# Kernel optimization log

Hardware: AMD Instinct MI355X
Metric: run time of the kernel (lower is better)

Reference implementation:

```python
import jax, jax.numpy as jnp
import numpy as np

B, S, H, R = 32, 512, 1024, 64


def _bernoulli(key, shape, p=0.05):
    return (jax.random.uniform(key, shape) < p).astype(jnp.float32)


def setup_inputs() -> dict:
    key = jax.random.key(0)
    ks = jax.random.split(key, 16)
    context = jax.random.normal(ks[0], (B, S, H), dtype=jnp.float32)
    masks = jnp.ones((B, S), dtype=jnp.float32)
    all_subject_heads = _bernoulli(ks[1], (B, S))
    all_subject_tails = _bernoulli(ks[2], (B, S))
    # one-hot subject head/tail positions (tail >= head)
    h_pos = jax.random.randint(ks[3], (B,), 0, S // 2)
    t_pos = h_pos + jax.random.randint(ks[4], (B,), 0, 8)
    subject_head = jax.nn.one_hot(h_pos, S, dtype=jnp.float32)
    subject_tail = jax.nn.one_hot(t_pos, S, dtype=jnp.float32)
    object_heads = _bernoulli(ks[5], (B, S, R))
    object_tails = _bernoulli(ks[6], (B, S, R))
    # learned parameters (PyTorch Linear: y = x @ W.T + b; store as [in, out])
    sc = 1.0 / np.sqrt(H)
    Ws_h = jax.random.uniform(ks[7], (H, 1), minval=-sc, maxval=sc)
    bs_h = jnp.zeros((1,), dtype=jnp.float32)
    Ws_t = jax.random.uniform(ks[8], (H, 1), minval=-sc, maxval=sc)
    bs_t = jnp.zeros((1,), dtype=jnp.float32)
    Wo_h = jax.random.uniform(ks[9], (H, R), minval=-sc, maxval=sc)
    bo_h = jnp.zeros((R,), dtype=jnp.float32)
    Wo_t = jax.random.uniform(ks[10], (H, R), minval=-sc, maxval=sc)
    bo_t = jnp.zeros((R,), dtype=jnp.float32)
    return dict(context=context, masks=masks,
                all_subject_heads=all_subject_heads, all_subject_tails=all_subject_tails,
                subject_head=subject_head, subject_tail=subject_tail,
                object_heads=object_heads, object_tails=object_tails,
                Ws_h=Ws_h, bs_h=bs_h, Ws_t=Ws_t, bs_t=bs_t,
                Wo_h=Wo_h, bo_h=bo_h, Wo_t=Wo_t, bo_t=bo_t)


def _bce_with_logits(logits, targets):
    # numerically stable, matches F.binary_cross_entropy_with_logits(reduction='none')
    return jnp.maximum(logits, 0.0) - logits * targets + jnp.log1p(jnp.exp(-jnp.abs(logits)))


def _masked_loss(gold, pred, mask):
    loss = _bce_with_logits(pred, gold)
    if loss.ndim != mask.ndim:
        mask = mask[..., None]
    return jnp.sum(loss * mask) / jnp.sum(mask)


def reference(context, masks, all_subject_heads, all_subject_tails,
              subject_head, subject_tail, object_heads, object_tails,
              Ws_h, bs_h, Ws_t, bs_t, Wo_h, bo_h, Wo_t, bo_t):
    # subject logits: [B,S]
    pred_subject_heads = (context @ Ws_h + bs_h)[..., 0]
    pred_subject_tails = (context @ Ws_t + bs_t)[..., 0]
    # subject pooling: one-hot [B,S] x context [B,S,H] -> [B,H]
    sub_h = jnp.einsum('bs,bsh->bh', subject_head, context)
    sub_t = jnp.einsum('bs,bsh->bh', subject_tail, context)
    subject = (sub_h + sub_t) * 0.5
    context_subject = context + subject[:, None, :]  # [B,S,H]
    pred_object_heads = context_subject @ Wo_h + bo_h  # [B,S,R]
    pred_object_tails = context_subject @ Wo_t + bo_t  # [B,S,R]
    loss = (_masked_loss(all_subject_heads, pred_subject_heads, masks)
            + _masked_loss(all_subject_tails, pred_subject_tails, masks)
            + _masked_loss(object_heads, pred_object_heads, masks)
            + _masked_loss(object_tails, pred_object_tails, masks))
    return loss
```

## Files before the change

### kernel.cpp

```cpp
#include <hip/hip_runtime.h>
#include <hip/hip_bf16.h>


#define B_  32
#define S_  512
#define H_  1024
#define R_  64
#define M_  (B_ * S_)
#define NPAD 160
#define NVALID 130
#define BK 64
#define BKP 72
#define MT 32

typedef __attribute__((ext_vector_type(4))) float  floatx4;
typedef __attribute__((ext_vector_type(8))) short  short8;
typedef __attribute__((ext_vector_type(4))) unsigned short u16x4;
typedef __attribute__((ext_vector_type(8))) unsigned short u16x8;

__device__ __forceinline__ unsigned short f2bf(float f) {
    unsigned int u = __float_as_uint(f);
    u = (u + 0x7FFFu + ((u >> 16) & 1u)) >> 16;
    return (unsigned short)u;
}
__device__ __forceinline__ float bf2f(unsigned short h) {
    return __uint_as_float(((unsigned int)h) << 16);
}

__global__ void prep_weights(const float* __restrict__ Wo_h,
                             const float* __restrict__ Wo_t,
                             const float* __restrict__ Ws_h,
                             const float* __restrict__ Ws_t,
                             unsigned short* __restrict__ WtG) {
    int n = blockIdx.x;
    int tid = threadIdx.x;
    for (int k = tid; k < H_; k += 256) {
        float v;
        if (n < 64)        v = Wo_h[k * R_ + n];
        else if (n < 128)  v = Wo_t[k * R_ + (n - 64)];
        else if (n == 128) v = Ws_h[k];
        else if (n == 129) v = Ws_t[k];
        else               v = 0.0f;
        WtG[n * H_ + k] = f2bf(v);
    }
}

__global__ __launch_bounds__(256) void subj_kernel(
        const float* __restrict__ ctx, const float* __restrict__ head,
        const float* __restrict__ tail, const float* __restrict__ masks,
        const float* __restrict__ Wo_h, const float* __restrict__ Wo_t,
        const float* __restrict__ bo_h, const float* __restrict__ bo_t,
        const float* __restrict__ bs_h, const float* __restrict__ bs_t,
        float* __restrict__ rowBias, float* __restrict__ accum) {
    int b = blockIdx.x, tid = threadIdx.x;
    __shared__ float subj[H_];
    __shared__ int cnt;
    __shared__ int   sidx[8];
    __shared__ float sw[8];
    if (tid == 0) cnt = 0;
    __syncthreads();
    float msk = 0.0f;
    for (int s = tid; s < S_; s += 256) {
        float w = 0.5f * (head[b * S_ + s] + tail[b * S_ + s]);
        if (w != 0.0f) {
            int i = atomicAdd(&cnt, 1);
            if (i < 8) { sidx[i] = s; sw[i] = w; }
        }
        msk += masks[b * S_ + s];
    }
    for (int o = 32; o > 0; o >>= 1) msk += __shfl_down(msk, o, 64);
    if ((tid & 63) == 0) atomicAdd(&accum[1], msk);
    __syncthreads();
    int nnz = cnt < 8 ? cnt : 8;
    for (int h = tid; h < H_; h += 256) {
        float a = 0.0f;
        for (int i = 0; i < nnz; i++)
            a += sw[i] * ctx[((size_t)b * S_ + sidx[i]) * H_ + h];
        subj[h] = a;
    }
    __syncthreads();
    if (tid < NPAD) {
        float bias = tid < 64  ? bo_h[tid]
                   : tid < 128 ? bo_t[tid - 64]
                   : tid == 128 ? bs_h[0]
                   : tid == 129 ? bs_t[0] : 0.0f;
        float acc2 = 0.0f;
        if (tid < 128) {
            const float* W = (tid < 64) ? Wo_h : Wo_t;
            int c = tid & 63;
            for (int k = 0; k < H_; k++) acc2 += subj[k] * W[k * R_ + c];
        }
        rowBias[b * NPAD + tid] = bias + acc2;
    }
}

__global__ __launch_bounds__(256, 2) void main_kernel(
        const float* __restrict__ ctx, const unsigned short* __restrict__ WtG,
        const float* __restrict__ rowBias, const float* __restrict__ masks,
        const float* __restrict__ ash, const float* __restrict__ ast,
        const float* __restrict__ oh, const float* __restrict__ ot,
        float* __restrict__ accum) {
    __shared__ __align__(16) unsigned short Asm[MT * BKP];
    __shared__ __align__(16) unsigned short Bsm[NPAD * BKP];
    __shared__ float rbuf[4];

    const int tid = threadIdx.x;
    const int bm = blockIdx.x;
    const int gm0 = bm * MT;
    const int b = gm0 >> 9;
    const int wave = tid >> 6, lane = tid & 63;
    const int wm = wave & 1;
    const int wn = wave >> 1;
    const int lr = lane & 15, q = lane >> 4;

    const int ar = tid >> 4, af = tid & 15;
    const int bn = tid >> 3, bf = tid & 7;
    const float* aSrc0 = ctx + (size_t)(gm0 + ar) * H_ + af * 4;
    const unsigned short* bSrc0 = WtG + bn * H_ + bf * 8;
    unsigned short* aDst0 = &Asm[ar * BKP + af * 4];
    unsigned short* bDst0 = &Bsm[bn * BKP + bf * 8];

    const int aOff = (wm * 16 + lr) * BKP + q * 8;
    const int bOffBase = (wn * 80 + lr) * BKP + q * 8;

    floatx4 acc[5];
#pragma unroll
    for (int t = 0; t < 5; t++) acc[t] = (floatx4){0.f, 0.f, 0.f, 0.f};

    for (int k0 = 0; k0 < H_; k0 += BK) {
        __syncthreads();
#pragma unroll
        for (int ii = 0; ii < 2; ii++) {
            const float4 v = *(const float4*)(aSrc0 + ii * 16 * H_ + k0);
            u16x4 u = { f2bf(v.x), f2bf(v.y), f2bf(v.z), f2bf(v.w) };
            *(u16x4*)(aDst0 + ii * 16 * BKP) = u;
        }
#pragma unroll
        for (int ii = 0; ii < 5; ii++) {
            u16x8 w = *(const u16x8*)(bSrc0 + ii * 32 * H_ + k0);
            *(u16x8*)(bDst0 + ii * 32 * BKP) = w;
        }
        __syncthreads();
#pragma unroll
        for (int kk = 0; kk < BK; kk += 32) {
            short8 afr = *(const short8*)&Asm[aOff + kk];
#pragma unroll
            for (int t = 0; t < 5; t++) {
                short8 bfr = *(const short8*)&Bsm[bOffBase + t * 16 * BKP + kk];
                acc[t] = __builtin_amdgcn_mfma_f32_16x16x32_bf16(afr, bfr, acc[t], 0, 0, 0);
            }
        }
    }

    float lsum = 0.0f;
#pragma unroll
    for (int t = 0; t < 5; t++) {
        const int col = wn * 80 + t * 16 + lr;
        if (col < NVALID) {
            const float rb = rowBias[b * NPAD + col];
#pragma unroll
            for (int i = 0; i < 4; i++) {
                const int row = gm0 + wm * 16 + q * 4 + i;
                const float l = acc[t][i] + rb;
                float tgt;
                if (col < 64)        tgt = oh[row * R_ + col];
                else if (col < 128)  tgt = ot[row * R_ + (col - 64)];
                else if (col == 128) tgt = ash[row];
                else                 tgt = ast[row];
                const float mk = masks[row];
                const float bce = fmaxf(l, 0.0f) - l * tgt + log1pf(__expf(-fabsf(l)));
                lsum += bce * mk;
            }
        }
    }
    for (int o = 32; o > 0; o >>= 1) lsum += __shfl_down(lsum, o, 64);
    if (lane == 0) rbuf[wave] = lsum;
    __syncthreads();
    if (tid == 0) atomicAdd(&accum[0], rbuf[0] + rbuf[1] + rbuf[2] + rbuf[3]);
}

__global__ void finalize_kernel(const float* __restrict__ accum, float* __restrict__ out) {
    out[0] = accum[0] / accum[1];
}

extern "C" void kernel_launch(void* const* d_in, const int* in_sizes, int n_in,
                              void* d_out, int out_size, void* d_ws, size_t ws_size,
                              hipStream_t stream) {
    const float* ctx   = (const float*)d_in[0];
    const float* masks = (const float*)d_in[1];
    const float* ash   = (const float*)d_in[2];
    const float* ast   = (const float*)d_in[3];
    const float* sh    = (const float*)d_in[4];
    const float* st    = (const float*)d_in[5];
    const float* oh    = (const float*)d_in[6];
    const float* ot    = (const float*)d_in[7];
    const float* Ws_h  = (const float*)d_in[8];
    const float* bs_h  = (const float*)d_in[9];
    const float* Ws_t  = (const float*)d_in[10];
    const float* bs_t  = (const float*)d_in[11];
    const float* Wo_h  = (const float*)d_in[12];
    const float* bo_h  = (const float*)d_in[13];
    const float* Wo_t  = (const float*)d_in[14];
    const float* bo_t  = (const float*)d_in[15];
    float* out = (float*)d_out;

    char* ws = (char*)d_ws;
    float* accum   = (float*)(ws + 0);
    float* rowBias = (float*)(ws + 256);
    unsigned short* WtG = (unsigned short*)(ws + 256 + 32 * NPAD * 4);

    hipMemsetAsync(accum, 0, 8, stream);
    prep_weights<<<NPAD, 256, 0, stream>>>(Wo_h, Wo_t, Ws_h, Ws_t, WtG);
    subj_kernel<<<B_, 256, 0, stream>>>(ctx, sh, st, masks, Wo_h, Wo_t,
                                        bo_h, bo_t, bs_h, bs_t, rowBias, accum);
    main_kernel<<<M_ / MT, 256, 0, stream>>>(ctx, WtG, rowBias, masks,
                                             ash, ast, oh, ot, accum);
    finalize_kernel<<<1, 1, 0, stream>>>(accum, out);
}
```

Before: 167.5 us.

## Split-K main GEMM across waves with 32x32 MFMA and fuse aux kernels

Merges weight prep and subject pooling into one aux kernel, and splits the rowBias dot product across two halves of the block. The main kernel drops LDS staging: each wave loads its K-quarter of A and B straight from global into registers, with software prefetch, and uses 32x32x16 bf16 MFMA. Partial sums from the four waves are reduced through LDS. A last-block atomic counter replaces the finalize kernel. This is meant to cut launch overhead and LDS sync cost, but it adds a large LDS reduction buffer, more register pressure, and uncoalesced-ish direct global loads.

```diff
diff --git a/kernel.cpp b/kernel.cpp
--- a/kernel.cpp
+++ b/kernel.cpp
@@ -1,5 +1,4 @@
 #include <hip/hip_runtime.h>
-#include <hip/hip_bf16.h>
 
 
 #define B_  32
@@ -9,54 +8,56 @@
 #define M_  (B_ * S_)
 #define NPAD 160
 #define NVALID 130
-#define BK 64
-#define BKP 72
-#define MT 32
-
-typedef __attribute__((ext_vector_type(4))) float  floatx4;
-typedef __attribute__((ext_vector_type(8))) short  short8;
-typedef __attribute__((ext_vector_type(4))) unsigned short u16x4;
-typedef __attribute__((ext_vector_type(8))) unsigned short u16x8;
+#define KW  256
+
+typedef __attribute__((ext_vector_type(4)))  float floatx4;
+typedef __attribute__((ext_vector_type(16))) float floatx16;
+typedef __attribute__((ext_vector_type(8)))  short short8;
 
 __device__ __forceinline__ unsigned short f2bf(float f) {
     unsigned int u = __float_as_uint(f);
     u = (u + 0x7FFFu + ((u >> 16) & 1u)) >> 16;
     return (unsigned short)u;
 }
-__device__ __forceinline__ float bf2f(unsigned short h) {
-    return __uint_as_float(((unsigned int)h) << 16);
-}
-
-__global__ void prep_weights(const float* __restrict__ Wo_h,
-                             const float* __restrict__ Wo_t,
-                             const float* __restrict__ Ws_h,
-                             const float* __restrict__ Ws_t,
-                             unsigned short* __restrict__ WtG) {
-    int n = blockIdx.x;
-    int tid = threadIdx.x;
-    for (int k = tid; k < H_; k += 256) {
-        float v;
-        if (n < 64)        v = Wo_h[k * R_ + n];
-        else if (n < 128)  v = Wo_t[k * R_ + (n - 64)];
-        else if (n == 128) v = Ws_h[k];
-        else if (n == 129) v = Ws_t[k];
-        else               v = 0.0f;
-        WtG[n * H_ + k] = f2bf(v);
-    }
-}
-
-__global__ __launch_bounds__(256) void subj_kernel(
+
+__device__ __forceinline__ short8 cvt8(float4 a, float4 b) {
+    union { unsigned short us[8]; short8 s8; } u;
+    u.us[0] = f2bf(a.x); u.us[1] = f2bf(a.y); u.us[2] = f2bf(a.z); u.us[3] = f2bf(a.w);
+    u.us[4] = f2bf(b.x); u.us[5] = f2bf(b.y); u.us[6] = f2bf(b.z); u.us[7] = f2bf(b.w);
+    return u.s8;
+}
+
+__global__ __launch_bounds__(256) void aux_kernel(
         const float* __restrict__ ctx, const float* __restrict__ head,
         const float* __restrict__ tail, const float* __restrict__ masks,
         const float* __restrict__ Wo_h, const float* __restrict__ Wo_t,
+        const float* __restrict__ Ws_h, const float* __restrict__ Ws_t,
         const float* __restrict__ bo_h, const float* __restrict__ bo_t,
         const float* __restrict__ bs_h, const float* __restrict__ bs_t,
-        float* __restrict__ rowBias, float* __restrict__ accum) {
-    int b = blockIdx.x, tid = threadIdx.x;
+        unsigned short* __restrict__ WtG, float* __restrict__ rowBias,
+        float* __restrict__ accum) {
+    const int tid = threadIdx.x;
     __shared__ float subj[H_];
+    __shared__ float part[256];
     __shared__ int cnt;
     __shared__ int   sidx[8];
     __shared__ float sw[8];
+
+    if (blockIdx.x < NPAD) {
+        const int n = blockIdx.x;
+        for (int k = tid; k < H_; k += 256) {
+            float v;
+            if (n < 64)        v = Wo_h[k * R_ + n];
+            else if (n < 128)  v = Wo_t[k * R_ + (n - 64)];
+            else if (n == 128) v = Ws_h[k];
+            else if (n == 129) v = Ws_t[k];
+            else               v = 0.0f;
+            WtG[n * H_ + k] = f2bf(v);
+        }
+        return;
+    }
+
+    const int b = blockIdx.x - NPAD;
     if (tid == 0) cnt = 0;
     __syncthreads();
     float msk = 0.0f;
@@ -71,7 +72,7 @@
     for (int o = 32; o > 0; o >>= 1) msk += __shfl_down(msk, o, 64);
     if ((tid & 63) == 0) atomicAdd(&accum[1], msk);
     __syncthreads();
-    int nnz = cnt < 8 ? cnt : 8;
+    const int nnz = cnt < 8 ? cnt : 8;
     for (int h = tid; h < H_; h += 256) {
         float a = 0.0f;
         for (int i = 0; i < nnz; i++)
@@ -79,18 +80,23 @@
         subj[h] = a;
     }
     __syncthreads();
+    {
+        const int c = tid & 127, half = tid >> 7;
+        const float* W = (c < 64) ? Wo_h : Wo_t;
+        const int cc = c & 63;
+        float a2 = 0.0f;
+        const int k0 = half * 512;
+        for (int k = k0; k < k0 + 512; ++k) a2 += subj[k] * W[k * R_ + cc];
+        part[tid] = a2;
+    }
+    __syncthreads();
     if (tid < NPAD) {
         float bias = tid < 64  ? bo_h[tid]
                    : tid < 128 ? bo_t[tid - 64]
                    : tid == 128 ? bs_h[0]
                    : tid == 129 ? bs_t[0] : 0.0f;
-        float acc2 = 0.0f;
-        if (tid < 128) {
-            const float* W = (tid < 64) ? Wo_h : Wo_t;
-            int c = tid & 63;
-            for (int k = 0; k < H_; k++) acc2 += subj[k] * W[k * R_ + c];
-        }
-        rowBias[b * NPAD + tid] = bias + acc2;
+        float a2 = (tid < 128) ? (part[tid] + part[tid + 128]) : 0.0f;
+        rowBias[b * NPAD + tid] = bias + a2;
     }
 }
 
@@ -99,88 +105,107 @@
         const float* __restrict__ rowBias, const float* __restrict__ masks,
         const float* __restrict__ ash, const float* __restrict__ ast,
         const float* __restrict__ oh, const float* __restrict__ ot,
-        float* __restrict__ accum) {
-    __shared__ __align__(16) unsigned short Asm[MT * BKP];
-    __shared__ __align__(16) unsigned short Bsm[NPAD * BKP];
-    __shared__ float rbuf[4];
-
-    const int tid = threadIdx.x;
-    const int bm = blockIdx.x;
-    const int gm0 = bm * MT;
-    const int b = gm0 >> 9;
+        float* __restrict__ accum, float* __restrict__ out) {
+    __shared__ float red[3 * 5 * 16 * 64];
+
+    const int tid  = threadIdx.x;
     const int wave = tid >> 6, lane = tid & 63;
-    const int wm = wave & 1;
-    const int wn = wave >> 1;
-    const int lr = lane & 15, q = lane >> 4;
-
-    const int ar = tid >> 4, af = tid & 15;
-    const int bn = tid >> 3, bf = tid & 7;
-    const float* aSrc0 = ctx + (size_t)(gm0 + ar) * H_ + af * 4;
-    const unsigned short* bSrc0 = WtG + bn * H_ + bf * 8;
-    unsigned short* aDst0 = &Asm[ar * BKP + af * 4];
-    unsigned short* bDst0 = &Bsm[bn * BKP + bf * 8];
-
-    const int aOff = (wm * 16 + lr) * BKP + q * 8;
-    const int bOffBase = (wn * 80 + lr) * BKP + q * 8;
-
-    floatx4 acc[5];
-#pragma unroll
-    for (int t = 0; t < 5; t++) acc[t] = (floatx4){0.f, 0.f, 0.f, 0.f};
-
-    for (int k0 = 0; k0 < H_; k0 += BK) {
-        __syncthreads();
-#pragma unroll
-        for (int ii = 0; ii < 2; ii++) {
-            const float4 v = *(const float4*)(aSrc0 + ii * 16 * H_ + k0);
-            u16x4 u = { f2bf(v.x), f2bf(v.y), f2bf(v.z), f2bf(v.w) };
-            *(u16x4*)(aDst0 + ii * 16 * BKP) = u;
-        }
-#pragma unroll
-        for (int ii = 0; ii < 5; ii++) {
-            u16x8 w = *(const u16x8*)(bSrc0 + ii * 32 * H_ + k0);
-            *(u16x8*)(bDst0 + ii * 32 * BKP) = w;
-        }
-        __syncthreads();
-#pragma unroll
-        for (int kk = 0; kk < BK; kk += 32) {
-            short8 afr = *(const short8*)&Asm[aOff + kk];
-#pragma unroll
-            for (int t = 0; t < 5; t++) {
-                short8 bfr = *(const short8*)&Bsm[bOffBase + t * 16 * BKP + kk];
-                acc[t] = __builtin_amdgcn_mfma_f32_16x16x32_bf16(afr, bfr, acc[t], 0, 0, 0);
+    const int r31  = lane & 31, q = lane >> 5;
+    const int gm0  = blockIdx.x * 32;
+    const int b    = gm0 >> 9;
+
+    const float*          aP = ctx + (size_t)(gm0 + r31) * H_ + wave * KW + q * 8;
+    const unsigned short* bP = WtG + (size_t)r31 * H_ + wave * KW + q * 8;
+
+    floatx16 acc[5];
+#pragma unroll
+    for (int t = 0; t < 5; ++t)
+#pragma unroll
+        for (int r = 0; r < 16; ++r) acc[t][r] = 0.0f;
+
+    float4 a0 = *(const float4*)(aP);
+    float4 a1 = *(const float4*)(aP + 4);
+    short8 bc[5];
+#pragma unroll
+    for (int t = 0; t < 5; ++t) bc[t] = *(const short8*)(bP + t * 32 * H_);
+
+#pragma unroll
+    for (int ks = 0; ks < 15; ++ks) {
+        float4 na0 = *(const float4*)(aP + (ks + 1) * 16);
+        float4 na1 = *(const float4*)(aP + (ks + 1) * 16 + 4);
+        short8 nb[5];
+#pragma unroll
+        for (int t = 0; t < 5; ++t)
+            nb[t] = *(const short8*)(bP + t * 32 * H_ + (ks + 1) * 16);
+        const short8 af = cvt8(a0, a1);
+#pragma unroll
+        for (int t = 0; t < 5; ++t)
+            acc[t] = __builtin_amdgcn_mfma_f32_32x32x16_bf16(af, bc[t], acc[t], 0, 0, 0);
+        a0 = na0; a1 = na1;
+#pragma unroll
+        for (int t = 0; t < 5; ++t) bc[t] = nb[t];
+    }
+    {
+        const short8 af = cvt8(a0, a1);
+#pragma unroll
+        for (int t = 0; t < 5; ++t)
+            acc[t] = __builtin_amdgcn_mfma_f32_32x32x16_bf16(af, bc[t], acc[t], 0, 0, 0);
+    }
+
+    if (wave > 0) {
+        float* dst = &red[(wave - 1) * 5120];
+#pragma unroll
+        for (int t = 0; t < 5; ++t)
+#pragma unroll
+            for (int r = 0; r < 16; ++r)
+                dst[(t * 16 + r) * 64 + lane] = acc[t][r];
+    }
+    __syncthreads();
+    if (wave == 0) {
+#pragma unroll
+        for (int t = 0; t < 5; ++t)
+#pragma unroll
+            for (int r = 0; r < 16; ++r) {
+                const int o = (t * 16 + r) * 64 + lane;
+                acc[t][r] += red[o] + red[o + 5120] + red[o + 10240];
             }
-        }
-    }
-
-    float lsum = 0.0f;
-#pragma unroll
-    for (int t = 0; t < 5; t++) {
-        const int col = wn * 80 + t * 16 + lr;
-        if (col < NVALID) {
+
+        float lsum = 0.0f;
+#pragma unroll
+        for (int t = 0; t < 5; ++t) {
+            const int col = t * 32 + r31;
             const float rb = rowBias[b * NPAD + col];
 #pragma unroll
-            for (int i = 0; i < 4; i++) {
-                const int row = gm0 + wm * 16 + q * 4 + i;
-                const float l = acc[t][i] + rb;
+            for (int r = 0; r < 16; ++r) {
+                const int row = gm0 + (r & 3) + 8 * (r >> 2) + 4 * q;
+                const float l = acc[t][r] + rb;
                 float tgt;
-                if (col < 64)        tgt = oh[row * R_ + col];
-                else if (col < 128)  tgt = ot[row * R_ + (col - 64)];
+                bool valid = true;
+                if (col < 64)        tgt = oh[(size_t)row * R_ + col];
+                else if (col < 128)  tgt = ot[(size_t)row * R_ + (col - 64)];
                 else if (col == 128) tgt = ash[row];
-                else                 tgt = ast[row];
-                const float mk = masks[row];
-                const float bce = fmaxf(l, 0.0f) - l * tgt + log1pf(__expf(-fabsf(l)));
-                lsum += bce * mk;
+                else if (col == 129) tgt = ast[row];
+                else                 valid = false;
+                if (valid) {
+                    const float mk = masks[row];
+                    const float bce = fmaxf(l, 0.0f) - l * tgt + log1pf(__expf(-fabsf(l)));
+                    lsum += bce * mk;
+                }
             }
         }
-    }
-    for (int o = 32; o > 0; o >>= 1) lsum += __shfl_down(lsum, o, 64);
-    if (lane == 0) rbuf[wave] = lsum;
-    __syncthreads();
-    if (tid == 0) atomicAdd(&accum[0], rbuf[0] + rbuf[1] + rbuf[2] + rbuf[3]);
-}
-
-__global__ void finalize_kernel(const float* __restrict__ accum, float* __restrict__ out) {
-    out[0] = accum[0] / accum[1];
+#pragma unroll
+        for (int o = 32; o > 0; o >>= 1) lsum += __shfl_down(lsum, o, 64);
+        if (lane == 0) {
+            atomicAdd(&accum[0], lsum);
+            __threadfence();
+            const unsigned int prev = atomicAdd((unsigned int*)(accum + 2), 1u);
+            if (prev == gridDim.x - 1) {
+                const float s = atomicAdd(&accum[0], 0.0f);
+                const float m = atomicAdd(&accum[1], 0.0f);
+                out[0] = s / m;
+            }
+        }
+    }
 }
 
 extern "C" void kernel_launch(void* const* d_in, const int* in_sizes, int n_in,
@@ -209,11 +234,10 @@
     float* rowBias = (float*)(ws + 256);
     unsigned short* WtG = (unsigned short*)(ws + 256 + 32 * NPAD * 4);
 
-    hipMemsetAsync(accum, 0, 8, stream);
-    prep_weights<<<NPAD, 256, 0, stream>>>(Wo_h, Wo_t, Ws_h, Ws_t, WtG);
-    subj_kernel<<<B_, 256, 0, stream>>>(ctx, sh, st, masks, Wo_h, Wo_t,
-                                        bo_h, bo_t, bs_h, bs_t, rowBias, accum);
-    main_kernel<<<M_ / MT, 256, 0, stream>>>(ctx, WtG, rowBias, masks,
-                                             ash, ast, oh, ot, accum);
-    finalize_kernel<<<1, 1, 0, stream>>>(accum, out);
-}
+    hipMemsetAsync(accum, 0, 12, stream);
+    aux_kernel<<<NPAD + B_, 256, 0, stream>>>(ctx, sh, st, masks, Wo_h, Wo_t,
+                                              Ws_h, Ws_t, bo_h, bo_t, bs_h, bs_t,
+                                              WtG, rowBias, accum);
+    main_kernel<<<M_ / 32, 256, 0, stream>>>(ctx, WtG, rowBias, masks,
+                                             ash, ast, oh, ot, accum, out);
+}
```

New measurement: 230.3 us. +37.5%, slower.
